# Kernel tuning notes

Hardware: AMD Instinct MI355X
Metric: run time of the kernel (lower is better)

## Reference

```python
import jax, jax.numpy as jnp
import numpy as np

EPS = 1e-5

def _bn(h, gamma, beta):
    # training-mode batch norm over dim 0 (biased variance, as torch)
    mu = h.mean(axis=0)
    var = ((h - mu) ** 2).mean(axis=0)
    return (h - mu) * jax.lax.rsqrt(var + EPS) * gamma + beta

def _mlp(h, W1, b1, g1, be1, W2, b2):
    # PyG MLP, num_layers=2: Linear -> BatchNorm -> ReLU -> Linear (dropout=0)
    h = h @ W1 + b1
    h = jax.nn.relu(_bn(h, g1, be1))
    return h @ W2 + b2

def setup_inputs() -> dict:
    key = jax.random.key(0)
    ks = jax.random.split(key, 12)
    N, E = 50000, 800000
    node_dim, edge_dim, hidden = 64, 64, 128
    d_in1 = node_dim + edge_dim   # 128
    d_in2 = node_dim + hidden     # 192
    def lin(k, fi, fo):
        s = 1.0 / np.sqrt(fi)
        return jax.random.uniform(k, (fi, fo), jnp.float32, -s, s)
    inp = {
        "x": jax.random.normal(ks[0], (N, node_dim), jnp.float32),
        "edge_index": jax.random.randint(ks[1], (2, E), 0, N, jnp.int32),
        "edge_attr": jax.random.normal(ks[2], (E, edge_dim), jnp.float32),
        "u": jax.random.normal(ks[3], (1, 16), jnp.float32),
        "batch": jnp.zeros((N,), jnp.int32),
        # node_mlp_1 params
        "W1a": lin(ks[4], d_in1, hidden), "b1a": jnp.zeros((hidden,), jnp.float32),
        "g1a": jnp.ones((hidden,), jnp.float32), "be1a": jnp.zeros((hidden,), jnp.float32),
        "W2a": lin(ks[5], hidden, hidden), "b2a": jnp.zeros((hidden,), jnp.float32),
        # node_mlp_2 params
        "W1b": lin(ks[6], d_in2, hidden), "b1b": jnp.zeros((hidden,), jnp.float32),
        "g1b": jnp.ones((hidden,), jnp.float32), "be1b": jnp.zeros((hidden,), jnp.float32),
        "W2b": lin(ks[7], hidden, node_dim), "b2b": jnp.zeros((node_dim,), jnp.float32),
    }
    return inp

def reference(x, edge_index, edge_attr, u, batch,
              W1a, b1a, g1a, be1a, W2a, b2a,
              W1b, b1b, g1b, be1b, W2b, b2b):
    row, col = edge_index[0], edge_index[1]
    # gather source nodes, concat edge features  -> [E, node_dim+edge_dim]
    out = jnp.concatenate([x[row], edge_attr], axis=1)
    out = _mlp(out, W1a, b1a, g1a, be1a, W2a, b2a)          # [E, hidden]
    out = jax.ops.segment_sum(out, col, num_segments=x.shape[0])  # scatter_add -> [N, hidden]
    out = jnp.concatenate([x, out], axis=1)                  # [N, node_dim+hidden]
    return _mlp(out, W1b, b1b, g1b, be1b, W2b, b2b)          # [N, node_dim]
```

## Files before the change

### kernel.cpp

```cpp
#include <hip/hip_runtime.h>
#include <hip/hip_fp16.h>


typedef _Float16 half8  __attribute__((ext_vector_type(8)));
typedef _Float16 half4h __attribute__((ext_vector_type(4)));
typedef float    floatx4 __attribute__((ext_vector_type(4)));

#define MFMA16(a, b, c) __builtin_amdgcn_mfma_f32_16x16x32_f16(a, b, c, 0, 0, 0)

#define LDS_BARRIER() do { \
    asm volatile("s_waitcnt lgkmcnt(0)" ::: "memory"); \
    __builtin_amdgcn_s_barrier(); \
} while (0)

__device__ __forceinline__ float col_reduce16(float v) {
    v += __shfl_xor(v, 16, 64);
    v += __shfl_xor(v, 32, 64);
    return v;
}

__global__ void k_prep(const float* __restrict__ w1a, const float* __restrict__ w2a,
                       const float* __restrict__ w1b, const float* __restrict__ w2b,
                       _Float16* __restrict__ w1at, _Float16* __restrict__ w2at,
                       _Float16* __restrict__ w1bt, _Float16* __restrict__ w2bt) {
    int i = blockIdx.x * 256 + threadIdx.x;
    if (i < 16384) {
        int n = i >> 7, k = i & 127;
        w1at[n * 128 + k] = (_Float16)w1a[k * 128 + n];
    } else if (i < 32768) {
        int j = i - 16384; int n = j >> 7, k = j & 127;
        w2at[n * 128 + k] = (_Float16)w2a[k * 128 + n];
    } else if (i < 57344) {
        int j = i - 32768; int n = j / 192, k = j - n * 192;
        w1bt[n * 192 + k] = (_Float16)w1b[k * 128 + n];
    } else if (i < 65536) {
        int j = i - 57344; int n = j >> 7, k = j & 127;
        w2bt[n * 128 + k] = (_Float16)w2b[k * 64 + n];
    }
}

__global__ void k_hist(const int* __restrict__ coli, int* __restrict__ cnt, int E) {
    int i = blockIdx.x * 512 + threadIdx.x;
    if (i < E) atomicAdd(&cnt[coli[i]], 1);
}

__global__ __launch_bounds__(1024) void k_scan(const int* __restrict__ cnt,
                                               int* __restrict__ cur, int N) {
    __shared__ int sp[1024];
    int t = threadIdx.x;
    int chunk = (N + 1023) >> 10;
    int base = t * chunk;
    int s = 0;
    for (int j = 0; j < chunk; j++) {
        int idx = base + j;
        if (idx < N) s += cnt[idx];
    }
    sp[t] = s; __syncthreads();
    for (int off = 1; off < 1024; off <<= 1) {
        int v = (t >= off) ? sp[t - off] : 0;
        __syncthreads();
        sp[t] += v;
        __syncthreads();
    }
    int run = sp[t] - s;
    for (int j = 0; j < chunk; j++) {
        int idx = base + j;
        if (idx < N) { cur[idx] = run; run += cnt[idx]; }
    }
}

__global__ void k_scatter(const int* __restrict__ rowi, const int* __restrict__ coli,
                          int* __restrict__ cur, int* __restrict__ rowp,
                          int* __restrict__ eidp, int* __restrict__ colp, int E) {
    int i = blockIdx.x * 512 + threadIdx.x;
    if (i < E) {
        int c = coli[i];
        int p = atomicAdd(&cur[c], 1);
        rowp[p] = rowi[i];
        eidp[p] = i;
        colp[p] = c;
    }
}

__global__ __launch_bounds__(512, 4) void k_edge_stats(
    const float* __restrict__ x, const int* __restrict__ rowi,
    const float* __restrict__ ea, const _Float16* __restrict__ w1t,
    float* __restrict__ gsum, float* __restrict__ gsq, int nTiles) {
    __shared__ _Float16 sW[128][136];
    __shared__ _Float16 sIn[128][136];
    const int tid = threadIdx.x, lane = tid & 63, wv = tid >> 6;
    const int lm = lane & 15, q = lane >> 4, koff = q * 8;
    const int G = gridDim.x;
    const int e = tid >> 2, part = tid & 3;

    {
        int n = tid >> 2, seg = (tid & 3) * 32;
        const half8* src = (const half8*)(w1t + n * 128 + seg);
        half8* dst = (half8*)&sW[n][seg];
        dst[0] = src[0]; dst[1] = src[1]; dst[2] = src[2]; dst[3] = src[3];
    }
    float sAcc[8], ssAcc[8];
#pragma unroll
    for (int i = 0; i < 8; i++) { sAcc[i] = 0.f; ssAcc[i] = 0.f; }

    int t = blockIdx.x;
    floatx4 pv[8];
    {
        long ge = (long)t * 128 + e;
        const float* src = (part < 2) ? x + (long)rowi[ge] * 64 + part * 32
                                      : ea + ge * 64 + (part - 2) * 32;
#pragma unroll
        for (int i = 0; i < 8; i++) pv[i] = ((const floatx4*)src)[i];
    }
    for (; t < nTiles; t += G) {
        {
            _Float16* dst = &sIn[e][part * 32];
#pragma unroll
            for (int i = 0; i < 8; i++) {
                half4h h = {(_Float16)pv[i][0], (_Float16)pv[i][1],
                            (_Float16)pv[i][2], (_Float16)pv[i][3]};
                *(half4h*)(dst + i * 4) = h;
            }
        }
        LDS_BARRIER();
        int tn = t + G;
        if (tn < nTiles) {
            long ge = (long)tn * 128 + e;
            const float* src = (part < 2) ? x + (long)rowi[ge] * 64 + part * 32
                                          : ea + ge * 64 + (part - 2) * 32;
#pragma unroll
            for (int i = 0; i < 8; i++) pv[i] = ((const floatx4*)src)[i];
        }
        half8 a[4];
#pragma unroll
        for (int kb = 0; kb < 4; kb++)
            a[kb] = *(const half8*)&sIn[wv * 16 + lm][kb * 32 + koff];
#pragma unroll
        for (int nt = 0; nt < 8; nt++) {
            floatx4 acc = {0.f, 0.f, 0.f, 0.f};
            const int c = nt * 16 + lm;
#pragma unroll
            for (int kb = 0; kb < 4; kb++) {
                half8 b = *(const half8*)&sW[c][kb * 32 + koff];
                acc = MFMA16(a[kb], b, acc);
            }
            sAcc[nt]  += acc[0] + acc[1] + acc[2] + acc[3];
            ssAcc[nt] += acc[0]*acc[0] + acc[1]*acc[1] + acc[2]*acc[2] + acc[3]*acc[3];
        }
        LDS_BARRIER();
    }
#pragma unroll
    for (int nt = 0; nt < 8; nt++) {
        float s  = col_reduce16(sAcc[nt]);
        float ss = col_reduce16(ssAcc[nt]);
        if (q == 0) {
            int c = nt * 16 + lm;
            int slot = (blockIdx.x * 8 + wv) & 15;
            unsafeAtomicAdd(&gsum[slot * 128 + c], s);
            unsafeAtomicAdd(&gsq[slot * 128 + c], ss);
        }
    }
}

__global__ void k_finalize(const float* __restrict__ sums, const float* __restrict__ sqs,
                           const float* __restrict__ gamma, const float* __restrict__ beta,
                           float* __restrict__ scale, float* __restrict__ shift, float count) {
    int i = threadIdx.x;
    float s = 0.f, ssq = 0.f;
    for (int j = 0; j < 16; j++) { s += sums[j * 128 + i]; ssq += sqs[j * 128 + i]; }
    float mu = s / count;
    float var = ssq / count - mu * mu;
    float sc = gamma[i] * rsqrtf(var + 1e-5f);
    scale[i] = sc;
    shift[i] = beta[i] - mu * sc;
}

__global__ __launch_bounds__(512, 2) void k_edge_mlp(
    const float* __restrict__ x, const int* __restrict__ rowp, const int* __restrict__ eidp,
    const int* __restrict__ colp,
    const float* __restrict__ ea, const _Float16* __restrict__ w1t, const _Float16* __restrict__ w2t,
    const float* __restrict__ scale, const float* __restrict__ shift, const float* __restrict__ b2a,
    __half* __restrict__ agg, int nTiles) {
    __shared__ _Float16 sW1[128][136];
    __shared__ _Float16 sW2[128][136];
    __shared__ _Float16 sIn[2][128][136];
    __shared__ float sScale[128], sShift[128], sB2[128];
    __shared__ int sCol[2][128];
    const int tid = threadIdx.x, lane = tid & 63, wv = tid >> 6;
    const int lm = lane & 15, q = lane >> 4, koff = q * 8;
    const int G = gridDim.x;
    const int e = tid >> 2, part = tid & 3;

    {
        int n = tid >> 2, seg = (tid & 3) * 32;
        const half8* s1 = (const half8*)(w1t + n * 128 + seg);
        half8* d1 = (half8*)&sW1[n][seg];
        d1[0] = s1[0]; d1[1] = s1[1]; d1[2] = s1[2]; d1[3] = s1[3];
        const half8* s2 = (const half8*)(w2t + n * 128 + seg);
        half8* d2 = (half8*)&sW2[n][seg];
        d2[0] = s2[0]; d2[1] = s2[1]; d2[2] = s2[2]; d2[3] = s2[3];
    }
    if (tid < 128) { sScale[tid] = scale[tid]; sShift[tid] = shift[tid]; sB2[tid] = b2a[tid]; }

    int t = blockIdx.x;
    {
        long ge = (long)t * 128 + e;
        int idx = (part < 2) ? rowp[ge] : eidp[ge];
        const float* src = (part < 2) ? x + (long)idx * 64 + part * 32
                                      : ea + (long)idx * 64 + (part - 2) * 32;
        _Float16* dst = &sIn[0][e][part * 32];
#pragma unroll
        for (int i = 0; i < 8; i++) {
            floatx4 v = ((const floatx4*)src)[i];
            half4h h = {(_Float16)v[0], (_Float16)v[1], (_Float16)v[2], (_Float16)v[3]};
            *(half4h*)(dst + i * 4) = h;
        }
        if (tid < 128) sCol[0][tid] = colp[(long)t * 128 + tid];
    }
    __syncthreads();
    int p = 0;
    for (; t < nTiles; t += G) {
        half8 a[4];
#pragma unroll
        for (int kb = 0; kb < 4; kb++)
            a[kb] = *(const half8*)&sIn[p][wv * 16 + lm][kb * 32 + koff];
        int myCol[4];
        const int m0 = wv * 16 + q * 4;
#pragma unroll
        for (int r = 0; r < 4; r++) myCol[r] = sCol[p][m0 + r];
        int cp = sCol[p][(q > 0) ? m0 - 1 : m0];
        int cn = sCol[p][(q < 3) ? m0 + 4 : m0 + 3];
        const bool h0 = (q == 0) || (myCol[0] != cp);
        const bool h1 = myCol[1] != myCol[0];
        const bool h2 = myCol[2] != myCol[1];
        const bool h3 = myCol[3] != myCol[2];
        const bool t0 = h1, t1 = h2, t2 = h3;
        const bool t3 = (q == 3) || (myCol[3] != cn);
        const bool c0m = !h0, c1m = c0m && !h1, c2m = c1m && !h2, c3m = c2m && !h3;
        const int F0 = (h0 | h1 | h2 | h3) ? 1 : 0;
        int Fp1 = __shfl(F0, (lane - 16) & 63, 64);
        const bool add1 = (q >= 1) && !F0;
        const int F1 = (F0 || ((q >= 1) && Fp1)) ? 1 : 0;
        const bool add2 = (q >= 2) && !F1;
        const bool useC = (q >= 1) && !h0;

        int tn = t + G; bool hasNext = tn < nTiles;
        floatx4 pv[8]; int pcol = 0;
        if (hasNext) {
            long ge = (long)tn * 128 + e;
            int idx = (part < 2) ? rowp[ge] : eidp[ge];
            const float* src = (part < 2) ? x + (long)idx * 64 + part * 32
                                          : ea + (long)idx * 64 + (part - 2) * 32;
#pragma unroll
            for (int i = 0; i < 8; i++) pv[i] = ((const floatx4*)src)[i];
            if (tid < 128) pcol = colp[(long)tn * 128 + tid];
        }
        floatx4 acc1[8];
#pragma unroll
        for (int nt = 0; nt < 8; nt++) {
            floatx4 acc = {0.f, 0.f, 0.f, 0.f};
            const int c = nt * 16 + lm;
#pragma unroll
            for (int kb = 0; kb < 4; kb++) {
                half8 b = *(const half8*)&sW1[c][kb * 32 + koff];
                acc = MFMA16(a[kb], b, acc);
            }
            acc1[nt] = acc;
        }
        LDS_BARRIER();

        _Float16(*sT)[136] = sIn[p];
#pragma unroll
        for (int nt = 0; nt < 8; nt++) {
            const int c = nt * 16 + lm;
            float sc = sScale[c], sh = sShift[c];
            half4h h;
#pragma unroll
            for (int r = 0; r < 4; r++)
                h[r] = (_Float16)fmaxf(acc1[nt][r] * sc + sh, 0.f);
            *(half4h*)&sT[c][wv * 16 + q * 4] = h;
        }
        half8 a2[4];
#pragma unroll
        for (int kb = 0; kb < 4; kb++) {
#pragma unroll
            for (int j = 0; j < 8; j++)
                a2[kb][j] = sT[kb * 32 + koff + j][wv * 16 + lm];
        }
#pragma unroll
        for (int nt = 0; nt < 8; nt++) {
            floatx4 acc = {0.f, 0.f, 0.f, 0.f};
            const int c = nt * 16 + lm;
#pragma unroll
            for (int kb = 0; kb < 4; kb++) {
                half8 b = *(const half8*)&sW2[c][kb * 32 + koff];
                acc = MFMA16(a2[kb], b, acc);
            }
            acc1[nt] = acc;
        }
        if (hasNext) {
            _Float16* dst = &sIn[p ^ 1][e][part * 32];
#pragma unroll
            for (int i = 0; i < 8; i++) {
                half4h h = {(_Float16)pv[i][0], (_Float16)pv[i][1],
                            (_Float16)pv[i][2], (_Float16)pv[i][3]};
                *(half4h*)(dst + i * 4) = h;
            }
            if (tid < 128) sCol[p ^ 1][tid] = pcol;
        }
#pragma unroll
        for (int nt = 0; nt < 8; nt++) {
            const int c = nt * 16 + lm;
            const int c0 = c & ~1;
            float bb = sB2[c];
            float v0 = acc1[nt][0] + bb, v1 = acc1[nt][1] + bb;
            float v2 = acc1[nt][2] + bb, v3 = acc1[nt][3] + bb;
            float s0 = v0;
            float s1 = h1 ? v1 : (s0 + v1);
            float s2 = h2 ? v2 : (s1 + v2);
            float s3 = h3 ? v3 : (s2 + v3);
            float S = s3;
            float Sp = __shfl(S, (lane - 16) & 63, 64);
            if (add1) S += Sp;
            float Sq = __shfl(S, (lane - 32) & 63, 64);
            if (add2) S += Sq;
            float Cc = __shfl(S, (lane - 16) & 63, 64);
            float C = useC ? Cc : 0.f;
            float f0 = c0m ? (s0 + C) : s0;
            float f1 = c1m ? (s1 + C) : s1;
            float f2 = c2m ? (s2 + C) : s2;
            float f3 = c3m ? (s3 + C) : s3;
            float g0 = __shfl_xor(f0, 1, 64), g1 = __shfl_xor(f1, 1, 64);
            float g2 = __shfl_xor(f2, 1, 64), g3 = __shfl_xor(f3, 1, 64);
            if ((lane & 1) == 0) {
                if (t0) unsafeAtomicAdd((__half2*)&agg[(size_t)myCol[0] * 128 + c0], __floats2half2_rn(f0, g0));
                if (t1) unsafeAtomicAdd((__half2*)&agg[(size_t)myCol[1] * 128 + c0], __floats2half2_rn(f1, g1));
            } else {
                if (t2) unsafeAtomicAdd((__half2*)&agg[(size_t)myCol[2] * 128 + c0], __floats2half2_rn(g2, f2));
                if (t3) unsafeAtomicAdd((__half2*)&agg[(size_t)myCol[3] * 128 + c0], __floats2half2_rn(g3, f3));
            }
        }
        LDS_BARRIER();
        p ^= 1;
    }
}

__global__ __launch_bounds__(512, 2) void k_node_a(
    const float* __restrict__ x, const __half* __restrict__ agg,
    const _Float16* __restrict__ w1bt, float* __restrict__ h3,
    float* __restrict__ gsum, float* __restrict__ gsq, int N) {
    __shared__ _Float16 sIn[128][200];
    __shared__ _Float16 sW[128][200];
    __shared__ float sSum[128], sSq[128];
    const int tid = threadIdx.x, lane = tid & 63, wv = tid >> 6;
    const long e0 = (long)blockIdx.x * 128;

    {
        int n = tid >> 2, seg = (tid & 3) * 48;
        const half8* src = (const half8*)(w1bt + n * 192 + seg);
        half8* dst = (half8*)&sW[n][seg];
        dst[0] = src[0]; dst[1] = src[1]; dst[2] = src[2];
        dst[3] = src[3]; dst[4] = src[4]; dst[5] = src[5];
    }
    if (tid < 128) { sSum[tid] = 0.f; sSq[tid] = 0.f; }
    {
        int m = tid >> 2, seg = tid & 3;
        long gm = e0 + m;
        bool valid = gm < N;
        const float* srcx = x + gm * 64 + seg * 16;
        _Float16* dstx = &sIn[m][seg * 16];
#pragma unroll
        for (int i = 0; i < 4; i++) {
            floatx4 v = {0.f, 0.f, 0.f, 0.f};
            if (valid) v = ((const floatx4*)srcx)[i];
            half4h h = {(_Float16)v[0], (_Float16)v[1], (_Float16)v[2], (_Float16)v[3]};
            *(half4h*)(dstx + i * 4) = h;
        }
        const _Float16* srca = (const _Float16*)agg + gm * 128 + seg * 32;
        _Float16* dsta = &sIn[m][64 + seg * 32];
#pragma unroll
        for (int i = 0; i < 4; i++) {
            half8 v = {0, 0, 0, 0, 0, 0, 0, 0};
            if (valid) v = ((const half8*)srca)[i];
            *(half8*)(dsta + i * 8) = v;
        }
    }
    __syncthreads();

    const int lm = lane & 15, q = lane >> 4, koff = q * 8;
    half8 a[6];
#pragma unroll
    for (int kb = 0; kb < 6; kb++)
        a[kb] = *(const half8*)&sIn[wv * 16 + lm][kb * 32 + koff];
#pragma unroll
    for (int nt = 0; nt < 8; nt++) {
        floatx4 acc = {0.f, 0.f, 0.f, 0.f};
        const int c = nt * 16 + lm;
#pragma unroll
        for (int kb = 0; kb < 6; kb++) {
            half8 b = *(const half8*)&sW[c][kb * 32 + koff];
            acc = MFMA16(a[kb], b, acc);
        }
        float s  = acc[0] + acc[1] + acc[2] + acc[3];
        float ss = acc[0]*acc[0] + acc[1]*acc[1] + acc[2]*acc[2] + acc[3]*acc[3];
        s = col_reduce16(s); ss = col_reduce16(ss);
        if (q == 0) { atomicAdd(&sSum[c], s); atomicAdd(&sSq[c], ss); }
#pragma unroll
        for (int r = 0; r < 4; r++) {
            int m2 = wv * 16 + q * 4 + r;
            long gm2 = e0 + m2;
            if (gm2 < N) h3[gm2 * 128 + c] = acc[r];
        }
    }
    __syncthreads();
    if (tid < 128) {
        int slot = blockIdx.x & 15;
        unsafeAtomicAdd(&gsum[slot * 128 + tid], sSum[tid]);
        unsafeAtomicAdd(&gsq[slot * 128 + tid], sSq[tid]);
    }
}

__global__ __launch_bounds__(512, 2) void k_node_b(
    const float* __restrict__ h3, const _Float16* __restrict__ w2bt,
    const float* __restrict__ scale, const float* __restrict__ shift,
    const float* __restrict__ b2b, float* __restrict__ out, int N) {
    __shared__ _Float16 sH[128][136];
    __shared__ _Float16 sW[64][136];
    const int tid = threadIdx.x, lane = tid & 63, wv = tid >> 6;
    const long e0 = (long)blockIdx.x * 128;

    {
        int n = tid >> 3, seg = (tid & 7) * 16;
        const half8* src = (const half8*)(w2bt + n * 128 + seg);
        half8* dst = (half8*)&sW[n][seg];
        dst[0] = src[0]; dst[1] = src[1];
    }
    {
        int m = tid >> 2, seg = (tid & 3) * 32;
        long gm = e0 + m;
        bool valid = gm < N;
        const float* src = h3 + gm * 128 + seg;
        _Float16* dst = &sH[m][seg];
#pragma unroll
        for (int i = 0; i < 8; i++) {
            floatx4 v = {0.f, 0.f, 0.f, 0.f};
            if (valid) v = ((const floatx4*)src)[i];
            floatx4 sc = ((const floatx4*)(scale + seg))[i];
            floatx4 sh = ((const floatx4*)(shift + seg))[i];
            half4h h;
#pragma unroll
            for (int j = 0; j < 4; j++)
                h[j] = (_Float16)fmaxf(v[j] * sc[j] + sh[j], 0.f);
            *(half4h*)(dst + i * 4) = h;
        }
    }
    __syncthreads();

    const int lm = lane & 15, q = lane >> 4, koff = q * 8;
    half8 a[4];
#pragma unroll
    for (int kb = 0; kb < 4; kb++)
        a[kb] = *(const half8*)&sH[wv * 16 + lm][kb * 32 + koff];
#pragma unroll
    for (int nt = 0; nt < 4; nt++) {
        floatx4 acc = {0.f, 0.f, 0.f, 0.f};
        const int c = nt * 16 + lm;
#pragma unroll
        for (int kb = 0; kb < 4; kb++) {
            half8 b = *(const half8*)&sW[c][kb * 32 + koff];
            acc = MFMA16(a[kb], b, acc);
        }
        float bb = b2b[c];
#pragma unroll
        for (int r = 0; r < 4; r++) {
            int m2 = wv * 16 + q * 4 + r;
            long gm2 = e0 + m2;
            if (gm2 < N) out[gm2 * 64 + c] = acc[r] + bb;
        }
    }
}

extern "C" void kernel_launch(void* const* d_in, const int* in_sizes, int n_in,
                              void* d_out, int out_size, void* d_ws, size_t ws_size,
                              hipStream_t stream) {
    const float* x    = (const float*)d_in[0];
    const int*   eidx = (const int*)d_in[1];
    const float* ea   = (const float*)d_in[2];
    const float* W1a  = (const float*)d_in[5];
    const float* g1a  = (const float*)d_in[7];
    const float* be1a = (const float*)d_in[8];
    const float* W2a  = (const float*)d_in[9];
    const float* b2a  = (const float*)d_in[10];
    const float* W1b  = (const float*)d_in[11];
    const float* g1b  = (const float*)d_in[13];
    const float* be1b = (const float*)d_in[14];
    const float* W2b  = (const float*)d_in[15];
    const float* b2b  = (const float*)d_in[16];
    const int N = in_sizes[0] / 64;
    const int E = in_sizes[2] / 64;
    const int* rowi = eidx;
    const int* coli = eidx + E;

    float* ws   = (float*)d_ws;
    __half* agg = (__half*)ws;
    float* h3   = ws + (size_t)N * 64;
    float* st   = h3 + (size_t)N * 128;
    float* sumE = st,        * sqE = st + 2048;
    float* sumN = st + 4096, * sqN = st + 6144;
    float* scE  = st + 8192, * shE = st + 8320;
    float* scN  = st + 8448, * shN = st + 8576;
    _Float16* wh   = (_Float16*)(st + 8704);
    _Float16* w1at = wh;
    _Float16* w2at = wh + 16384;
    _Float16* w1bt = wh + 32768;
    _Float16* w2bt = wh + 57344;
    int* cnt  = (int*)(wh + 65536);
    int* cur  = cnt + N;
    int* rowp = cur + N;
    int* eidp = rowp + E;
    int* colp = eidp + E;

    hipMemsetAsync(agg, 0, (size_t)N * 128 * sizeof(__half), stream);
    hipMemsetAsync(st, 0, 8192 * sizeof(float), stream);
    hipMemsetAsync(cnt, 0, (size_t)N * sizeof(int), stream);
    k_prep<<<256, 256, 0, stream>>>(W1a, W2a, W1b, W2b, w1at, w2at, w1bt, w2bt);

    int nbE = (E + 511) / 512;
    k_hist<<<nbE, 512, 0, stream>>>(coli, cnt, E);
    k_scan<<<1, 1024, 0, stream>>>(cnt, cur, N);
    k_scatter<<<nbE, 512, 0, stream>>>(rowi, coli, cur, rowp, eidp, colp, E);

    int nTilesE = E / 128;
    int nbl = (N + 127) / 128;
    k_edge_stats<<<500, 512, 0, stream>>>(x, rowi, ea, w1at, sumE, sqE, nTilesE);
    k_finalize<<<1, 128, 0, stream>>>(sumE, sqE, g1a, be1a, scE, shE, (float)E);
    k_edge_mlp<<<250, 512, 0, stream>>>(x, rowp, eidp, colp, ea, w1at, w2at, scE, shE, b2a, agg, nTilesE);
    k_node_a<<<nbl, 512, 0, stream>>>(x, agg, w1bt, h3, sumN, sqN, N);
    k_finalize<<<1, 128, 0, stream>>>(sumN, sqN, g1b, be1b, scN, shN, (float)N);
    k_node_b<<<nbl, 512, 0, stream>>>(h3, w2bt, scN, shN, b2b, (float*)d_out, N);
}
```

Before: 742.3 us.

## Load edge inputs directly into MFMA fragments, dropping LDS staging and block barriers

Both edge kernels now gather `x` and `edge_attr` rows straight into registers in the MFMA A-operand layout, converting them to fp16 in registers. This removes the shared-memory input tiles and the block-wide barriers per tile. Destination column indices are loaded as an int4 per lane, and neighbour columns come from wave shuffles instead of LDS. The transpose buffer is now per-wave, so no cross-wave synchronisation is needed. Grid sizes move to 512 and 256 blocks. The cost is less coalesced global loads (32-byte chunks per lane), in exchange for lower LDS traffic and better overlap between waves.

```diff
diff --git a/kernel.cpp b/kernel.cpp
--- a/kernel.cpp
+++ b/kernel.cpp
@@ -8,10 +8,8 @@
 
 #define MFMA16(a, b, c) __builtin_amdgcn_mfma_f32_16x16x32_f16(a, b, c, 0, 0, 0)
 
-#define LDS_BARRIER() do { \
-    asm volatile("s_waitcnt lgkmcnt(0)" ::: "memory"); \
-    __builtin_amdgcn_s_barrier(); \
-} while (0)
+#define CVT8(lo, hi) (half8){(_Float16)(lo)[0], (_Float16)(lo)[1], (_Float16)(lo)[2], (_Float16)(lo)[3], \
+                             (_Float16)(hi)[0], (_Float16)(hi)[1], (_Float16)(hi)[2], (_Float16)(hi)[3]}
 
 __device__ __forceinline__ float col_reduce16(float v) {
     v += __shfl_xor(v, 16, 64);
@@ -87,11 +85,10 @@
     const float* __restrict__ ea, const _Float16* __restrict__ w1t,
     float* __restrict__ gsum, float* __restrict__ gsq, int nTiles) {
     __shared__ _Float16 sW[128][136];
-    __shared__ _Float16 sIn[128][136];
     const int tid = threadIdx.x, lane = tid & 63, wv = tid >> 6;
     const int lm = lane & 15, q = lane >> 4, koff = q * 8;
     const int G = gridDim.x;
-    const int e = tid >> 2, part = tid & 3;
+    const int row = wv * 16 + lm;
 
     {
         int n = tid >> 2, seg = (tid & 3) * 32;
@@ -99,6 +96,8 @@
         half8* dst = (half8*)&sW[n][seg];
         dst[0] = src[0]; dst[1] = src[1]; dst[2] = src[2]; dst[3] = src[3];
     }
+    __syncthreads();
+
     float sAcc[8], ssAcc[8];
 #pragma unroll
     for (int i = 0; i < 8; i++) { sAcc[i] = 0.f; ssAcc[i] = 0.f; }
@@ -106,35 +105,28 @@
     int t = blockIdx.x;
     floatx4 pv[8];
     {
-        long ge = (long)t * 128 + e;
-        const float* src = (part < 2) ? x + (long)rowi[ge] * 64 + part * 32
-                                      : ea + ge * 64 + (part - 2) * 32;
-#pragma unroll
-        for (int i = 0; i < 8; i++) pv[i] = ((const floatx4*)src)[i];
+        long ge = (long)t * 128 + row;
+        const float* px = x + (long)rowi[ge] * 64 + koff;
+        const float* pe = ea + ge * 64 + koff;
+        pv[0] = *(const floatx4*)(px);      pv[1] = *(const floatx4*)(px + 4);
+        pv[2] = *(const floatx4*)(px + 32); pv[3] = *(const floatx4*)(px + 36);
+        pv[4] = *(const floatx4*)(pe);      pv[5] = *(const floatx4*)(pe + 4);
+        pv[6] = *(const floatx4*)(pe + 32); pv[7] = *(const floatx4*)(pe + 36);
     }
     for (; t < nTiles; t += G) {
-        {
-            _Float16* dst = &sIn[e][part * 32];
-#pragma unroll
-            for (int i = 0; i < 8; i++) {
-                half4h h = {(_Float16)pv[i][0], (_Float16)pv[i][1],
-                            (_Float16)pv[i][2], (_Float16)pv[i][3]};
-                *(half4h*)(dst + i * 4) = h;
-            }
-        }
-        LDS_BARRIER();
+        half8 a[4];
+        a[0] = CVT8(pv[0], pv[1]); a[1] = CVT8(pv[2], pv[3]);
+        a[2] = CVT8(pv[4], pv[5]); a[3] = CVT8(pv[6], pv[7]);
         int tn = t + G;
         if (tn < nTiles) {
-            long ge = (long)tn * 128 + e;
-            const float* src = (part < 2) ? x + (long)rowi[ge] * 64 + part * 32
-                                          : ea + ge * 64 + (part - 2) * 32;
-#pragma unroll
-            for (int i = 0; i < 8; i++) pv[i] = ((const floatx4*)src)[i];
-        }
-        half8 a[4];
-#pragma unroll
-        for (int kb = 0; kb < 4; kb++)
-            a[kb] = *(const half8*)&sIn[wv * 16 + lm][kb * 32 + koff];
+            long ge = (long)tn * 128 + row;
+            const float* px = x + (long)rowi[ge] * 64 + koff;
+            const float* pe = ea + ge * 64 + koff;
+            pv[0] = *(const floatx4*)(px);      pv[1] = *(const floatx4*)(px + 4);
+            pv[2] = *(const floatx4*)(px + 32); pv[3] = *(const floatx4*)(px + 36);
+            pv[4] = *(const floatx4*)(pe);      pv[5] = *(const floatx4*)(pe + 4);
+            pv[6] = *(const floatx4*)(pe + 32); pv[7] = *(const floatx4*)(pe + 36);
+        }
 #pragma unroll
         for (int nt = 0; nt < 8; nt++) {
             floatx4 acc = {0.f, 0.f, 0.f, 0.f};
@@ -147,7 +139,6 @@
             sAcc[nt]  += acc[0] + acc[1] + acc[2] + acc[3];
             ssAcc[nt] += acc[0]*acc[0] + acc[1]*acc[1] + acc[2]*acc[2] + acc[3]*acc[3];
         }
-        LDS_BARRIER();
     }
 #pragma unroll
     for (int nt = 0; nt < 8; nt++) {
@@ -183,13 +174,13 @@
     __half* __restrict__ agg, int nTiles) {
     __shared__ _Float16 sW1[128][136];
     __shared__ _Float16 sW2[128][136];
-    __shared__ _Float16 sIn[2][128][136];
+    __shared__ _Float16 sT[128][136];
     __shared__ float sScale[128], sShift[128], sB2[128];
-    __shared__ int sCol[2][128];
     const int tid = threadIdx.x, lane = tid & 63, wv = tid >> 6;
     const int lm = lane & 15, q = lane >> 4, koff = q * 8;
     const int G = gridDim.x;
-    const int e = tid >> 2, part = tid & 3;
+    const int row = wv * 16 + lm;
+    const int m0 = wv * 16 + q * 4;
 
     {
         int n = tid >> 2, seg = (tid & 3) * 32;
@@ -201,35 +192,27 @@
         d2[0] = s2[0]; d2[1] = s2[1]; d2[2] = s2[2]; d2[3] = s2[3];
     }
     if (tid < 128) { sScale[tid] = scale[tid]; sShift[tid] = shift[tid]; sB2[tid] = b2a[tid]; }
+    __syncthreads();
 
     int t = blockIdx.x;
-    {
-        long ge = (long)t * 128 + e;
-        int idx = (part < 2) ? rowp[ge] : eidp[ge];
-        const float* src = (part < 2) ? x + (long)idx * 64 + part * 32
-                                      : ea + (long)idx * 64 + (part - 2) * 32;
-        _Float16* dst = &sIn[0][e][part * 32];
-#pragma unroll
-        for (int i = 0; i < 8; i++) {
-            floatx4 v = ((const floatx4*)src)[i];
-            half4h h = {(_Float16)v[0], (_Float16)v[1], (_Float16)v[2], (_Float16)v[3]};
-            *(half4h*)(dst + i * 4) = h;
-        }
-        if (tid < 128) sCol[0][tid] = colp[(long)t * 128 + tid];
-    }
-    __syncthreads();
-    int p = 0;
+    floatx4 pv[8]; int4 pcol;
+    {
+        long ge = (long)t * 128 + row;
+        const float* px = x + (long)rowp[ge] * 64 + koff;
+        const float* pe = ea + (long)eidp[ge] * 64 + koff;
+        pv[0] = *(const floatx4*)(px);      pv[1] = *(const floatx4*)(px + 4);
+        pv[2] = *(const floatx4*)(px + 32); pv[3] = *(const floatx4*)(px + 36);
+        pv[4] = *(const floatx4*)(pe);      pv[5] = *(const floatx4*)(pe + 4);
+        pv[6] = *(const floatx4*)(pe + 32); pv[7] = *(const floatx4*)(pe + 36);
+        pcol = *(const int4*)&colp[(long)t * 128 + m0];
+    }
     for (; t < nTiles; t += G) {
         half8 a[4];
-#pragma unroll
-        for (int kb = 0; kb < 4; kb++)
-            a[kb] = *(const half8*)&sIn[p][wv * 16 + lm][kb * 32 + koff];
-        int myCol[4];
-        const int m0 = wv * 16 + q * 4;
-#pragma unroll
-        for (int r = 0; r < 4; r++) myCol[r] = sCol[p][m0 + r];
-        int cp = sCol[p][(q > 0) ? m0 - 1 : m0];
-        int cn = sCol[p][(q < 3) ? m0 + 4 : m0 + 3];
+        a[0] = CVT8(pv[0], pv[1]); a[1] = CVT8(pv[2], pv[3]);
+        a[2] = CVT8(pv[4], pv[5]); a[3] = CVT8(pv[6], pv[7]);
+        int myCol[4] = {pcol.x, pcol.y, pcol.z, pcol.w};
+        int cp = __shfl(myCol[3], (lane - 16) & 63, 64);
+        int cn = __shfl(myCol[0], (lane + 16) & 63, 64);
         const bool h0 = (q == 0) || (myCol[0] != cp);
         const bool h1 = myCol[1] != myCol[0];
         const bool h2 = myCol[2] != myCol[1];
@@ -245,15 +228,15 @@
         const bool useC = (q >= 1) && !h0;
 
         int tn = t + G; bool hasNext = tn < nTiles;
-        floatx4 pv[8]; int pcol = 0;
         if (hasNext) {
-            long ge = (long)tn * 128 + e;
-            int idx = (part < 2) ? rowp[ge] : eidp[ge];
-            const float* src = (part < 2) ? x + (long)idx * 64 + part * 32
-                                          : ea + (long)idx * 64 + (part - 2) * 32;
-#pragma unroll
-            for (int i = 0; i < 8; i++) pv[i] = ((const floatx4*)src)[i];
-            if (tid < 128) pcol = colp[(long)tn * 128 + tid];
+            long ge = (long)tn * 128 + row;
+            const float* px = x + (long)rowp[ge] * 64 + koff;
+            const float* pe = ea + (long)eidp[ge] * 64 + koff;
+            pv[0] = *(const floatx4*)(px);      pv[1] = *(const floatx4*)(px + 4);
+            pv[2] = *(const floatx4*)(px + 32); pv[3] = *(const floatx4*)(px + 36);
+            pv[4] = *(const floatx4*)(pe);      pv[5] = *(const floatx4*)(pe + 4);
+            pv[6] = *(const floatx4*)(pe + 32); pv[7] = *(const floatx4*)(pe + 36);
+            pcol = *(const int4*)&colp[(long)tn * 128 + m0];
         }
         floatx4 acc1[8];
 #pragma unroll
@@ -267,9 +250,6 @@
             }
             acc1[nt] = acc;
         }
-        LDS_BARRIER();
-
-        _Float16(*sT)[136] = sIn[p];
 #pragma unroll
         for (int nt = 0; nt < 8; nt++) {
             const int c = nt * 16 + lm;
@@ -278,14 +258,14 @@
 #pragma unroll
             for (int r = 0; r < 4; r++)
                 h[r] = (_Float16)fmaxf(acc1[nt][r] * sc + sh, 0.f);
-            *(half4h*)&sT[c][wv * 16 + q * 4] = h;
+            *(half4h*)&sT[c][m0] = h;
         }
         half8 a2[4];
 #pragma unroll
         for (int kb = 0; kb < 4; kb++) {
 #pragma unroll
             for (int j = 0; j < 8; j++)
-                a2[kb][j] = sT[kb * 32 + koff + j][wv * 16 + lm];
+                a2[kb][j] = sT[kb * 32 + koff + j][row];
         }
 #pragma unroll
         for (int nt = 0; nt < 8; nt++) {
@@ -297,16 +277,6 @@
                 acc = MFMA16(a2[kb], b, acc);
             }
             acc1[nt] = acc;
-        }
-        if (hasNext) {
-            _Float16* dst = &sIn[p ^ 1][e][part * 32];
-#pragma unroll
-            for (int i = 0; i < 8; i++) {
-                half4h h = {(_Float16)pv[i][0], (_Float16)pv[i][1],
-                            (_Float16)pv[i][2], (_Float16)pv[i][3]};
-                *(half4h*)(dst + i * 4) = h;
-            }
-            if (tid < 128) sCol[p ^ 1][tid] = pcol;
         }
 #pragma unroll
         for (int nt = 0; nt < 8; nt++) {
@@ -340,8 +310,6 @@
                 if (t3) unsafeAtomicAdd((__half2*)&agg[(size_t)myCol[3] * 128 + c0], __floats2half2_rn(g3, f3));
             }
         }
-        LDS_BARRIER();
-        p ^= 1;
     }
 }
 
@@ -532,9 +500,9 @@
 
     int nTilesE = E / 128;
     int nbl = (N + 127) / 128;
-    k_edge_stats<<<500, 512, 0, stream>>>(x, rowi, ea, w1at, sumE, sqE, nTilesE);
+    k_edge_stats<<<512, 512, 0, stream>>>(x, rowi, ea, w1at, sumE, sqE, nTilesE);
     k_finalize<<<1, 128, 0, stream>>>(sumE, sqE, g1a, be1a, scE, shE, (float)E);
-    k_edge_mlp<<<250, 512, 0, stream>>>(x, rowp, eidp, colp, ea, w1at, w2at, scE, shE, b2a, agg, nTilesE);
+    k_edge_mlp<<<256, 512, 0, stream>>>(x, rowp, eidp, colp, ea, w1at, w2at, scE, shE, b2a, agg, nTilesE);
     k_node_a<<<nbl, 512, 0, stream>>>(x, agg, w1bt, h3, sumN, sqN, N);
     k_finalize<<<1, 128, 0, stream>>>(sumN, sqN, g1b, be1b, scN, shN, (float)N);
     k_node_b<<<nbl, 512, 0, stream>>>(h3, w2bt, scN, shN, b2b, (float*)d_out, N);
```

Result: slower. 1.175 ms (+58.3%).

## Fuse histogram into edge stats, pack CSR arrays into int2, fold finalize

Applied to the files above, without the earlier changes.

The destination-count histogram moves into the edge statistics kernel, which already streams the edge list, so the separate histogram pass goes away. The BN finalize runs inside the scatter kernel. The three permuted index arrays (row, edge id, col) become one int2 per edge, with col and row packed into 16-bit halves of one word, which cuts index traffic and launches. Grid sizes also move from 500/250 to 512/256. The packing assumes node ids fit in 16 bits, and N=50000 does fit.

```diff
diff --git a/kernel.cpp b/kernel.cpp
--- a/kernel.cpp
+++ b/kernel.cpp
@@ -39,11 +39,6 @@
     }
 }
 
-__global__ void k_hist(const int* __restrict__ coli, int* __restrict__ cnt, int E) {
-    int i = blockIdx.x * 512 + threadIdx.x;
-    if (i < E) atomicAdd(&cnt[coli[i]], 1);
-}
-
 __global__ __launch_bounds__(1024) void k_scan(const int* __restrict__ cnt,
                                                int* __restrict__ cur, int N) {
     __shared__ int sp[1024];
@@ -69,23 +64,36 @@
     }
 }
 
-__global__ void k_scatter(const int* __restrict__ rowi, const int* __restrict__ coli,
-                          int* __restrict__ cur, int* __restrict__ rowp,
-                          int* __restrict__ eidp, int* __restrict__ colp, int E) {
+__global__ void k_scatter_fin(const int* __restrict__ rowi, const int* __restrict__ coli,
+                              int* __restrict__ cur, int2* __restrict__ pairs,
+                              const float* __restrict__ sums, const float* __restrict__ sqs,
+                              const float* __restrict__ gamma, const float* __restrict__ beta,
+                              float* __restrict__ scale, float* __restrict__ shift,
+                              float count, int E) {
     int i = blockIdx.x * 512 + threadIdx.x;
     if (i < E) {
         int c = coli[i];
         int p = atomicAdd(&cur[c], 1);
-        rowp[p] = rowi[i];
-        eidp[p] = i;
-        colp[p] = c;
+        pairs[p] = make_int2(i, (c << 16) | rowi[i]);
+    }
+    if (blockIdx.x == 0 && threadIdx.x < 128) {
+        int j = threadIdx.x;
+        float s = 0.f, ssq = 0.f;
+        for (int k = 0; k < 16; k++) { s += sums[k * 128 + j]; ssq += sqs[k * 128 + j]; }
+        float mu = s / count;
+        float var = ssq / count - mu * mu;
+        float sc = gamma[j] * rsqrtf(var + 1e-5f);
+        scale[j] = sc;
+        shift[j] = beta[j] - mu * sc;
     }
 }
 
 __global__ __launch_bounds__(512, 4) void k_edge_stats(
     const float* __restrict__ x, const int* __restrict__ rowi,
+    const int* __restrict__ coli,
     const float* __restrict__ ea, const _Float16* __restrict__ w1t,
-    float* __restrict__ gsum, float* __restrict__ gsq, int nTiles) {
+    float* __restrict__ gsum, float* __restrict__ gsq,
+    int* __restrict__ cnt, int nTiles) {
     __shared__ _Float16 sW[128][136];
     __shared__ _Float16 sIn[128][136];
     const int tid = threadIdx.x, lane = tid & 63, wv = tid >> 6;
@@ -105,12 +113,14 @@
 
     int t = blockIdx.x;
     floatx4 pv[8];
+    int hc = 0;
     {
         long ge = (long)t * 128 + e;
         const float* src = (part < 2) ? x + (long)rowi[ge] * 64 + part * 32
                                       : ea + ge * 64 + (part - 2) * 32;
 #pragma unroll
         for (int i = 0; i < 8; i++) pv[i] = ((const floatx4*)src)[i];
+        if (part == 0) hc = coli[ge];
     }
     for (; t < nTiles; t += G) {
         {
@@ -123,6 +133,7 @@
             }
         }
         LDS_BARRIER();
+        if (part == 0) atomicAdd(&cnt[hc], 1);
         int tn = t + G;
         if (tn < nTiles) {
             long ge = (long)tn * 128 + e;
@@ -130,6 +141,7 @@
                                           : ea + ge * 64 + (part - 2) * 32;
 #pragma unroll
             for (int i = 0; i < 8; i++) pv[i] = ((const floatx4*)src)[i];
+            if (part == 0) hc = coli[ge];
         }
         half8 a[4];
 #pragma unroll
@@ -176,8 +188,7 @@
 }
 
 __global__ __launch_bounds__(512, 2) void k_edge_mlp(
-    const float* __restrict__ x, const int* __restrict__ rowp, const int* __restrict__ eidp,
-    const int* __restrict__ colp,
+    const float* __restrict__ x, const int2* __restrict__ pairs,
     const float* __restrict__ ea, const _Float16* __restrict__ w1t, const _Float16* __restrict__ w2t,
     const float* __restrict__ scale, const float* __restrict__ shift, const float* __restrict__ b2a,
     __half* __restrict__ agg, int nTiles) {
@@ -205,9 +216,9 @@
     int t = blockIdx.x;
     {
         long ge = (long)t * 128 + e;
-        int idx = (part < 2) ? rowp[ge] : eidp[ge];
-        const float* src = (part < 2) ? x + (long)idx * 64 + part * 32
-                                      : ea + (long)idx * 64 + (part - 2) * 32;
+        int2 pr = pairs[ge];
+        const float* src = (part < 2) ? x + (long)(pr.y & 0xFFFF) * 64 + part * 32
+                                      : ea + (long)pr.x * 64 + (part - 2) * 32;
         _Float16* dst = &sIn[0][e][part * 32];
 #pragma unroll
         for (int i = 0; i < 8; i++) {
@@ -215,7 +226,7 @@
             half4h h = {(_Float16)v[0], (_Float16)v[1], (_Float16)v[2], (_Float16)v[3]};
             *(half4h*)(dst + i * 4) = h;
         }
-        if (tid < 128) sCol[0][tid] = colp[(long)t * 128 + tid];
+        if (tid < 128) sCol[0][tid] = (int)(((unsigned)pairs[(long)t * 128 + tid].y) >> 16);
     }
     __syncthreads();
     int p = 0;
@@ -248,12 +259,12 @@
         floatx4 pv[8]; int pcol = 0;
         if (hasNext) {
             long ge = (long)tn * 128 + e;
-            int idx = (part < 2) ? rowp[ge] : eidp[ge];
-            const float* src = (part < 2) ? x + (long)idx * 64 + part * 32
-                                          : ea + (long)idx * 64 + (part - 2) * 32;
+            int2 pr = pairs[ge];
+            const float* src = (part < 2) ? x + (long)(pr.y & 0xFFFF) * 64 + part * 32
+                                          : ea + (long)pr.x * 64 + (part - 2) * 32;
 #pragma unroll
             for (int i = 0; i < 8; i++) pv[i] = ((const floatx4*)src)[i];
-            if (tid < 128) pcol = colp[(long)tn * 128 + tid];
+            if (tid < 128) pcol = (int)(((unsigned)pairs[(long)tn * 128 + tid].y) >> 16);
         }
         floatx4 acc1[8];
 #pragma unroll
@@ -516,25 +527,21 @@
     _Float16* w2bt = wh + 57344;
     int* cnt  = (int*)(wh + 65536);
     int* cur  = cnt + N;
-    int* rowp = cur + N;
-    int* eidp = rowp + E;
-    int* colp = eidp + E;
+    int2* pairs = (int2*)(cur + N);
 
     hipMemsetAsync(agg, 0, (size_t)N * 128 * sizeof(__half), stream);
     hipMemsetAsync(st, 0, 8192 * sizeof(float), stream);
     hipMemsetAsync(cnt, 0, (size_t)N * sizeof(int), stream);
     k_prep<<<256, 256, 0, stream>>>(W1a, W2a, W1b, W2b, w1at, w2at, w1bt, w2bt);
 
-    int nbE = (E + 511) / 512;
-    k_hist<<<nbE, 512, 0, stream>>>(coli, cnt, E);
-    k_scan<<<1, 1024, 0, stream>>>(cnt, cur, N);
-    k_scatter<<<nbE, 512, 0, stream>>>(rowi, coli, cur, rowp, eidp, colp, E);
-
     int nTilesE = E / 128;
     int nbl = (N + 127) / 128;
-    k_edge_stats<<<500, 512, 0, stream>>>(x, rowi, ea, w1at, sumE, sqE, nTilesE);
-    k_finalize<<<1, 128, 0, stream>>>(sumE, sqE, g1a, be1a, scE, shE, (float)E);
-    k_edge_mlp<<<250, 512, 0, stream>>>(x, rowp, eidp, colp, ea, w1at, w2at, scE, shE, b2a, agg, nTilesE);
+    int nbE = (E + 511) / 512;
+    k_edge_stats<<<512, 512, 0, stream>>>(x, rowi, coli, ea, w1at, sumE, sqE, cnt, nTilesE);
+    k_scan<<<1, 1024, 0, stream>>>(cnt, cur, N);
+    k_scatter_fin<<<nbE, 512, 0, stream>>>(rowi, coli, cur, pairs, sumE, sqE, g1a, be1a,
+                                           scE, shE, (float)E, E);
+    k_edge_mlp<<<256, 512, 0, stream>>>(x, pairs, ea, w1at, w2at, scE, shE, b2a, agg, nTilesE);
     k_node_a<<<nbl, 512, 0, stream>>>(x, agg, w1bt, h3, sumN, sqN, N);
     k_finalize<<<1, 128, 0, stream>>>(sumN, sqN, g1b, be1b, scN, shN, (float)N);
     k_node_b<<<nbl, 512, 0, stream>>>(h3, w2bt, scN, shN, b2b, (float*)d_out, N);
```

Measured after the change: 733.0 us. About the same (-1.3%).
